# Kernel tuning notes

Hardware: AMD Instinct MI355X
Metric: run time of the kernel (lower is better)

Reference implementation:

```python
import jax, jax.numpy as jnp
import numpy as np

S = 4096   # sequence length == max_length
L = 16     # CHAR_LENGTH
F = 256    # char feature size == word-embed size (hidden_size kwarg)
H = 512    # LSTM hidden = 2 * hidden_size kwarg
V = 44     # char vocab from build_char_lang()


def setup_inputs() -> dict:
    key = jax.random.key(0)
    ks = jax.random.split(key, 12)
    def rn(k, shape, s=0.05):
        return jax.random.normal(k, shape, jnp.float32) * s
    return {
        "word_embeddings": rn(ks[0], (S, F), 1.0),
        "char_idxs": jax.random.randint(ks[1], (S, L), 0, V),
        "char_embed": rn(ks[2], (V, F), 1.0),
        "conv_w": rn(ks[3], (F, 2, F)),           # [out_ch, kh=2, kw=F]
        "conv_b": jnp.zeros((F,), jnp.float32),
        "lin_w": rn(ks[4], (F, F)),
        "lin_b": jnp.zeros((F,), jnp.float32),
        "Wih_f": rn(ks[5], (4 * H, H)),
        "Whh_f": rn(ks[6], (4 * H, H)),
        "bih_f": jnp.zeros((4 * H,), jnp.float32),
        "bhh_f": jnp.zeros((4 * H,), jnp.float32),
        "Wih_r": rn(ks[7], (4 * H, H)),
        "Whh_r": rn(ks[8], (4 * H, H)),
        "bih_r": jnp.zeros((4 * H,), jnp.float32),
        "bhh_r": jnp.zeros((4 * H,), jnp.float32),
    }


def _lstm(x, Wih, Whh, bih, bhh):
    """PyTorch-convention single-layer LSTM over leading axis of x [T, H]."""
    Hh = Whh.shape[1]
    b = bih + bhh
    def step(carry, xt):
        h, c = carry
        g = xt @ Wih.T + h @ Whh.T + b          # [4H]
        i, f, gg, o = jnp.split(g, 4)
        c = jax.nn.sigmoid(f) * c + jax.nn.sigmoid(i) * jnp.tanh(gg)
        h = jax.nn.sigmoid(o) * jnp.tanh(c)
        return (h, c), h
    z = jnp.zeros((Hh,), x.dtype)
    (h, c), ys = jax.lax.scan(step, (z, z), x)
    return ys, h, c


def _char_cnn(char_idxs, char_embed, conv_w, conv_b, lin_w, lin_b):
    ce = char_embed[char_idxs]                          # [S, L, F]
    win = jnp.stack([ce[:, :-1, :], ce[:, 1:, :]], 2)    # [S, L-1, 2, F]
    conv = jnp.einsum('slkf,okf->slo', win, conv_w) + conv_b  # [S, L-1, F]
    pooled = jnp.max(jax.nn.relu(conv), axis=1)          # maxpool over L-1 -> [S, F]
    return pooled @ lin_w.T + lin_b                      # [S, F]


def reference(word_embeddings, char_idxs, char_embed, conv_w, conv_b, lin_w, lin_b,
              Wih_f, Whh_f, bih_f, bhh_f, Wih_r, Whh_r, bih_r, bhh_r):
    char_feat = _char_cnn(char_idxs, char_embed, conv_w, conv_b, lin_w, lin_b)
    x = jnp.concatenate([word_embeddings, char_feat], axis=1)   # [S, H]
    fwd_out, hf, cf = _lstm(x, Wih_f, Whh_f, bih_f, bhh_f)
    rev_out, hr, cr = _lstm(x[::-1], Wih_r, Whh_r, bih_r, bhh_r)
    outputs = jnp.concatenate([fwd_out, rev_out[::-1]], axis=1)  # [S, 2H]
    hidden = jnp.concatenate([hf, hr])                           # [2H]
    cell = jnp.concatenate([cf, cr])                             # [2H]
    return outputs, hidden, cell
```

## Files before the change

### kernel.cpp

```cpp
#include <hip/hip_runtime.h>
#include <cstdint>

#define SQ 4096
#define FD 256
#define HD 512
#define GD 2048

#define WS_X       0
#define WS_XPROJ   (WS_X + SQ*HD)
#define WS_WT      (WS_XPROJ + 2*SQ*GD)
#define WS_LINT    (WS_WT + 2*FD*FD)
#define WS_SYNC    (WS_LINT + FD*FD)

typedef __attribute__((ext_vector_type(4))) float f32x4;
typedef unsigned long long u64;

__device__ __forceinline__ float sigf(float x) { return 1.f / (1.f + __expf(-x)); }

#define REP32(M) M(0)M(1)M(2)M(3)M(4)M(5)M(6)M(7)M(8)M(9)M(10)M(11)M(12)M(13)M(14)M(15) \
                 M(16)M(17)M(18)M(19)M(20)M(21)M(22)M(23)M(24)M(25)M(26)M(27)M(28)M(29)M(30)M(31)

__global__ __launch_bounds__(256) void prep_kernel(const float* __restrict__ conv_w,
                                                   const float* __restrict__ lin_w,
                                                   float* __restrict__ Wt,
                                                   float* __restrict__ linT,
                                                   float* __restrict__ sync) {
  int n = blockIdx.x * 256 + threadIdx.x;
  if (n < 4096) sync[n] = 0.f;
  if (n < 2 * FD * FD) {
    int o = n & 255, f = (n >> 8) & 255, k = n >> 16;
    Wt[n] = conv_w[o * 512 + k * 256 + f];
  } else {
    int m = n - 2 * FD * FD;
    int o = m & 255, f = m >> 8;
    linT[m] = lin_w[o * 256 + f];
  }
}

__global__ __launch_bounds__(256) void charcnn_kernel(const float* __restrict__ wemb,
    const int* __restrict__ cidx, const float* __restrict__ cemb,
    const float* __restrict__ Wt, const float* __restrict__ conv_b,
    const float* __restrict__ linT, const float* __restrict__ lin_b,
    float* __restrict__ x) {
  __shared__ float ceT[256][20];
  __shared__ float pooled[256];
  int s = blockIdx.x, o = threadIdx.x;
  #pragma unroll
  for (int l = 0; l < 16; ++l) {
    int idx = cidx[s * 16 + l];
    ceT[o][l] = cemb[idx * 256 + o];
  }
  __syncthreads();
  float acc[15];
  float cb = conv_b[o];
  #pragma unroll
  for (int l = 0; l < 15; ++l) acc[l] = cb;
  for (int f = 0; f < 256; ++f) {
    float w0 = Wt[f * 256 + o];
    float w1 = Wt[65536 + f * 256 + o];
    float4 ca = *(const float4*)&ceT[f][0];
    float4 cv = *(const float4*)&ceT[f][4];
    float4 cc = *(const float4*)&ceT[f][8];
    float4 cd = *(const float4*)&ceT[f][12];
    float c[16] = {ca.x, ca.y, ca.z, ca.w, cv.x, cv.y, cv.z, cv.w,
                   cc.x, cc.y, cc.z, cc.w, cd.x, cd.y, cd.z, cd.w};
    #pragma unroll
    for (int l = 0; l < 15; ++l) acc[l] += c[l] * w0 + c[l + 1] * w1;
  }
  float m = 0.f;
  #pragma unroll
  for (int l = 0; l < 15; ++l) m = fmaxf(m, acc[l]);
  pooled[o] = m;
  __syncthreads();
  float a2 = lin_b[o];
  for (int f = 0; f < 256; f += 4) {
    float4 p = *(const float4*)&pooled[f];
    a2 += p.x * linT[(f + 0) * 256 + o] + p.y * linT[(f + 1) * 256 + o]
        + p.z * linT[(f + 2) * 256 + o] + p.w * linT[(f + 3) * 256 + o];
  }
  x[(size_t)s * 512 + o] = wemb[(size_t)s * 256 + o];
  x[(size_t)s * 512 + 256 + o] = a2;
}

__global__ __launch_bounds__(256) void xproj_kernel(const float* __restrict__ x,
    const float* __restrict__ Wih_f, const float* __restrict__ Wih_r,
    const float* __restrict__ bih_f, const float* __restrict__ bhh_f,
    const float* __restrict__ bih_r, const float* __restrict__ bhh_r,
    float* __restrict__ xproj) {
  __shared__ float As[64][33];
  __shared__ float Bs[64][33];
  int dir = blockIdx.z;
  const float* B  = dir ? Wih_r : Wih_f;
  const float* b1 = dir ? bih_r : bih_f;
  const float* b2 = dir ? bhh_r : bhh_f;
  int m0 = blockIdx.x * 64, n0 = blockIdx.y * 64;
  int tid = threadIdx.x, tx = tid & 15, ty = tid >> 4;
  float acc[4][4];
  #pragma unroll
  for (int j = 0; j < 4; ++j) {
    float bias = b1[n0 + tx * 4 + j] + b2[n0 + tx * 4 + j];
    #pragma unroll
    for (int i = 0; i < 4; ++i) acc[i][j] = bias;
  }
  int lc = tid & 31, lr0 = tid >> 5;
  for (int k0 = 0; k0 < 512; k0 += 32) {
    #pragma unroll
    for (int i = 0; i < 8; ++i) {
      As[lr0 + 8 * i][lc] = x[(size_t)(m0 + lr0 + 8 * i) * 512 + k0 + lc];
      Bs[lr0 + 8 * i][lc] = B[(size_t)(n0 + lr0 + 8 * i) * 512 + k0 + lc];
    }
    __syncthreads();
    #pragma unroll
    for (int kk = 0; kk < 32; ++kk) {
      float a0 = As[ty * 4 + 0][kk], a1 = As[ty * 4 + 1][kk];
      float a2 = As[ty * 4 + 2][kk], a3 = As[ty * 4 + 3][kk];
      float q0 = Bs[tx * 4 + 0][kk], q1 = Bs[tx * 4 + 1][kk];
      float q2 = Bs[tx * 4 + 2][kk], q3 = Bs[tx * 4 + 3][kk];
      acc[0][0] += a0 * q0; acc[0][1] += a0 * q1; acc[0][2] += a0 * q2; acc[0][3] += a0 * q3;
      acc[1][0] += a1 * q0; acc[1][1] += a1 * q1; acc[1][2] += a1 * q2; acc[1][3] += a1 * q3;
      acc[2][0] += a2 * q0; acc[2][1] += a2 * q1; acc[2][2] += a2 * q2; acc[2][3] += a2 * q3;
      acc[3][0] += a3 * q0; acc[3][1] += a3 * q1; acc[3][2] += a3 * q2; acc[3][3] += a3 * q3;
    }
    __syncthreads();
  }
  size_t base = (size_t)dir * SQ * GD;
  #pragma unroll
  for (int i = 0; i < 4; ++i) {
    float4 v = make_float4(acc[i][0], acc[i][1], acc[i][2], acc[i][3]);
    *(float4*)&xproj[base + (size_t)(m0 + ty * 4 + i) * GD + n0 + tx * 4] = v;
  }
}

__global__ __launch_bounds__(512, 2) void lstm_kernel(const float* __restrict__ xproj,
    const float* __restrict__ Whh_f, const float* __restrict__ Whh_r,
    u64* __restrict__ payu, float* __restrict__ out) {
  __shared__ float h4[4 * 132];
  __shared__ float g_lds[128];
  int dir = blockIdx.x >> 4;
  int wid = blockIdx.x & 15;
  int hbase = wid * 32;
  int tid = threadIdx.x;

  int r = tid >> 2, kq = tid & 3;
  int Rrow = ((r >> 5) << 9) + hbase + (r & 31);
  const float* Whh = dir ? Whh_r : Whh_f;
  const float* xp = xproj + (size_t)dir * SQ * GD;
  const f32x4* wsrc4 = (const f32x4*)(Whh + (size_t)Rrow * 512 + kq * 128);
#define LDW(i) f32x4 w##i = wsrc4[i];
  REP32(LDW)
#undef LDW

  int ib = tid >> 4, ic = tid & 15;
  float cst = 0.f, hlast = 0.f;

  for (int t = 0; t < SQ; ++t) {
    int p = dir ? (SQ - 1 - t) : t;
    float xval = 0.f;
    if (kq == 0) xval = xp[(size_t)p * GD + Rrow];
    if (tid < 256) {
      float v0, v1;
      if (t == 0) { v0 = 0.f; v1 = 0.f; }
      else {
        const u64* src = payu + ((((size_t)dir * 2 + ((t - 1) & 1)) * 16 + ib) * 16 + ic) * 2;
        unsigned tg = (unsigned)t;
        for (;;) {
          u64 lo = __hip_atomic_load(src,     __ATOMIC_RELAXED, __HIP_MEMORY_SCOPE_AGENT);
          u64 hi = __hip_atomic_load(src + 1, __ATOMIC_RELAXED, __HIP_MEMORY_SCOPE_AGENT);
          if ((unsigned)lo == tg && (unsigned)(hi >> 32) == tg) {
            v0 = __uint_as_float((unsigned)(lo >> 32));
            v1 = __uint_as_float((unsigned)hi);
            break;
          }
          __builtin_amdgcn_s_sleep(1);
        }
      }
      int ih = ib * 32 + ic * 2;
      h4[(ih >> 7) * 132 + (ih & 127)] = v0;
      int ih1 = ih + 1;
      h4[(ih1 >> 7) * 132 + (ih1 & 127)] = v1;
    }
    __syncthreads();
    float a0 = 0.f, a1 = 0.f, a2 = 0.f, a3 = 0.f;
    const f32x4* hq4 = (const f32x4*)&h4[kq * 132];
#define GST(i) { f32x4 hh = hq4[i]; \
    a0 = fmaf(w##i[0], hh[0], a0); a1 = fmaf(w##i[1], hh[1], a1); \
    a2 = fmaf(w##i[2], hh[2], a2); a3 = fmaf(w##i[3], hh[3], a3); }
    REP32(GST)
#undef GST
    float acc = (a0 + a1) + (a2 + a3);
    acc += __shfl_xor(acc, 1);
    acc += __shfl_xor(acc, 2);
    if (kq == 0) g_lds[r] = acc + xval;
    __syncthreads();
    if (tid < 32) {
      float ig = g_lds[tid], fg = g_lds[32 + tid], gg = g_lds[64 + tid], og = g_lds[96 + tid];
      float c = sigf(fg) * cst + sigf(ig) * tanhf(gg);
      float hval = sigf(og) * tanhf(c);
      cst = c; hlast = hval;
      out[(size_t)p * 1024 + dir * 512 + hbase + tid] = hval;
      unsigned tg = (unsigned)(t + 1);
      u64 word = (tid & 1) ? (((u64)tg << 32) | __float_as_uint(hval))
                           : (((u64)__float_as_uint(hval) << 32) | tg);
      u64* dst = payu + ((((size_t)dir * 2 + (t & 1)) * 16 + wid) * 16 + (tid >> 1)) * 2 + (tid & 1);
      __hip_atomic_store(dst, word, __ATOMIC_RELAXED, __HIP_MEMORY_SCOPE_AGENT);
    }
  }
  if (tid < 32) {
    size_t OH = (size_t)SQ * 1024;
    out[OH + dir * 512 + hbase + tid] = hlast;
    out[OH + 1024 + dir * 512 + hbase + tid] = cst;
  }
}

extern "C" void kernel_launch(void* const* d_in, const int* in_sizes, int n_in,
                              void* d_out, int out_size, void* d_ws, size_t ws_size,
                              hipStream_t stream) {
  const float* wemb   = (const float*)d_in[0];
  const int*   cidx   = (const int*)d_in[1];
  const float* cemb   = (const float*)d_in[2];
  const float* conv_w = (const float*)d_in[3];
  const float* conv_b = (const float*)d_in[4];
  const float* lin_w  = (const float*)d_in[5];
  const float* lin_b  = (const float*)d_in[6];
  const float* Wih_f  = (const float*)d_in[7];
  const float* Whh_f  = (const float*)d_in[8];
  const float* bih_f  = (const float*)d_in[9];
  const float* bhh_f  = (const float*)d_in[10];
  const float* Wih_r  = (const float*)d_in[11];
  const float* Whh_r  = (const float*)d_in[12];
  const float* bih_r  = (const float*)d_in[13];
  const float* bhh_r  = (const float*)d_in[14];
  float* out = (float*)d_out;
  float* ws = (float*)d_ws;
  float* x     = ws + WS_X;
  float* xproj = ws + WS_XPROJ;
  float* Wt    = ws + WS_WT;
  float* linT  = ws + WS_LINT;
  float* sync  = ws + WS_SYNC;

  prep_kernel<<<768, 256, 0, stream>>>(conv_w, lin_w, Wt, linT, sync);
  charcnn_kernel<<<SQ, 256, 0, stream>>>(wemb, cidx, cemb, Wt, conv_b, linT, lin_b, x);
  xproj_kernel<<<dim3(64, 32, 2), 256, 0, stream>>>(x, Wih_f, Wih_r, bih_f, bhh_f, bih_r, bhh_r, xproj);
  lstm_kernel<<<32, 512, 0, stream>>>(xproj, Whh_f, Whh_r, (u64*)sync, out);
}
```

Before: 8.594 ms.

## Replicate LSTM hidden-state mailbox per reader and split gate activations across lanes

Each producer block now writes its hidden-state words into 16 per-reader copies of the mailbox instead of one, so the reading blocks poll distinct cache lines rather than all contending on the same ones. The sleep in the poll loop is removed, mailbox addresses are precomputed outside the time loop, and the weight loads use inline assembly followed by an explicit wait. The gate nonlinearities are spread over 64 lanes with shuffles to shorten the serial tail of each step. The cost is 16 times more atomic stores per step, a larger sync region to zero, and busier spinning that may consume memory bandwidth.

```diff
diff --git a/kernel.cpp b/kernel.cpp
--- a/kernel.cpp
+++ b/kernel.cpp
@@ -26,7 +26,7 @@
                                                    float* __restrict__ linT,
                                                    float* __restrict__ sync) {
   int n = blockIdx.x * 256 + threadIdx.x;
-  if (n < 4096) sync[n] = 0.f;
+  if (n < 65536) sync[n] = 0.f;
   if (n < 2 * FD * FD) {
     int o = n & 255, f = (n >> 8) & 255, k = n >> 16;
     Wt[n] = conv_w[o * 512 + k * 256 + f];
@@ -146,11 +146,22 @@
   const float* Whh = dir ? Whh_r : Whh_f;
   const float* xp = xproj + (size_t)dir * SQ * GD;
   const f32x4* wsrc4 = (const f32x4*)(Whh + (size_t)Rrow * 512 + kq * 128);
-#define LDW(i) f32x4 w##i = wsrc4[i];
+#define LDW(i) f32x4 w##i; \
+  asm volatile("global_load_dwordx4 %0, %1, off offset:%2" \
+               : "=v"(w##i) : "v"(wsrc4), "i"(16 * i));
   REP32(LDW)
 #undef LDW
+  asm volatile("s_waitcnt vmcnt(0)" ::: "memory");
+  __builtin_amdgcn_sched_barrier(0);
 
   int ib = tid >> 4, ic = tid & 15;
+  size_t rd_off = (((size_t)wid * 16 + ib) * 16 + ic) * 2;
+  const u64* rd_base0 = payu + (size_t)(dir * 2 + 0) * 8192 + rd_off;
+  const u64* rd_base1 = payu + (size_t)(dir * 2 + 1) * 8192 + rd_off;
+  size_t wr_off = ((size_t)wid * 16 + (tid >> 1)) * 2 + (tid & 1);
+  u64* wr_base0 = payu + (size_t)(dir * 2 + 0) * 8192 + wr_off;
+  u64* wr_base1 = payu + (size_t)(dir * 2 + 1) * 8192 + wr_off;
+
   float cst = 0.f, hlast = 0.f;
 
   for (int t = 0; t < SQ; ++t) {
@@ -161,7 +172,7 @@
       float v0, v1;
       if (t == 0) { v0 = 0.f; v1 = 0.f; }
       else {
-        const u64* src = payu + ((((size_t)dir * 2 + ((t - 1) & 1)) * 16 + ib) * 16 + ic) * 2;
+        const u64* src = ((t - 1) & 1) ? rd_base1 : rd_base0;
         unsigned tg = (unsigned)t;
         for (;;) {
           u64 lo = __hip_atomic_load(src,     __ATOMIC_RELAXED, __HIP_MEMORY_SCOPE_AGENT);
@@ -171,7 +182,6 @@
             v1 = __uint_as_float((unsigned)hi);
             break;
           }
-          __builtin_amdgcn_s_sleep(1);
         }
       }
       int ih = ib * 32 + ic * 2;
@@ -192,17 +202,28 @@
     acc += __shfl_xor(acc, 2);
     if (kq == 0) g_lds[r] = acc + xval;
     __syncthreads();
-    if (tid < 32) {
-      float ig = g_lds[tid], fg = g_lds[32 + tid], gg = g_lds[64 + tid], og = g_lds[96 + tid];
-      float c = sigf(fg) * cst + sigf(ig) * tanhf(gg);
-      float hval = sigf(og) * tanhf(c);
-      cst = c; hlast = hval;
-      out[(size_t)p * 1024 + dir * 512 + hbase + tid] = hval;
-      unsigned tg = (unsigned)(t + 1);
-      u64 word = (tid & 1) ? (((u64)tg << 32) | __float_as_uint(hval))
-                           : (((u64)__float_as_uint(hval) << 32) | tg);
-      u64* dst = payu + ((((size_t)dir * 2 + (t & 1)) * 16 + wid) * 16 + (tid >> 1)) * 2 + (tid & 1);
-      __hip_atomic_store(dst, word, __ATOMIC_RELAXED, __HIP_MEMORY_SCOPE_AGENT);
+    if (tid < 64) {
+      int j = tid & 31;
+      bool hiw = tid >= 32;
+      float vA = hiw ? g_lds[64 + j] : g_lds[j];
+      float vB = hiw ? g_lds[96 + j] : g_lds[32 + j];
+      float aA = hiw ? tanhf(vA) : sigf(vA);
+      float aB = sigf(vB);
+      float bA = __shfl_xor(aA, 32);
+      float bB = __shfl_xor(aB, 32);
+      if (!hiw) {
+        float c = aB * cst + aA * bA;
+        float hval = bB * tanhf(c);
+        cst = c; hlast = hval;
+        unsigned tg = (unsigned)(t + 1);
+        u64 word = (tid & 1) ? (((u64)tg << 32) | __float_as_uint(hval))
+                             : (((u64)__float_as_uint(hval) << 32) | tg);
+        u64* wb = (t & 1) ? wr_base1 : wr_base0;
+        #pragma unroll
+        for (int rd = 0; rd < 16; ++rd)
+          __hip_atomic_store(wb + (size_t)rd * 512, word, __ATOMIC_RELAXED, __HIP_MEMORY_SCOPE_AGENT);
+        out[(size_t)p * 1024 + dir * 512 + hbase + tid] = hval;
+      }
     }
   }
   if (tid < 32) {
```

After: 10.54 ms. +22.6%, slower.

## Restructure LSTM step: per-lane gate mapping, shuffle gate gather, double-buffered h

Applied to the files above, without the earlier changes.

Remaps threads so each hidden unit's four gates sit in one wave, letting gate values be gathered with shuffles instead of an LDS round trip and a second barrier. It double-buffers the h vector in shared memory, publishes one tagged 64-bit word per hidden unit, and has all 512 threads poll without sleep. It also swaps tanhf for a fast exp-based approximation. Whh weights are now reloaded from global/L2 inside every timestep instead of being held in registers, which adds memory traffic per step.

```diff
diff --git a/kernel.cpp b/kernel.cpp
--- a/kernel.cpp
+++ b/kernel.cpp
@@ -16,6 +16,11 @@
 typedef unsigned long long u64;
 
 __device__ __forceinline__ float sigf(float x) { return 1.f / (1.f + __expf(-x)); }
+__device__ __forceinline__ float tanhf_fast(float x) {
+  float xx = fminf(15.f, fmaxf(-15.f, x));
+  float e = __expf(2.f * xx);
+  return (e - 1.f) * __frcp_rn(e + 1.f);
+}
 
 #define REP32(M) M(0)M(1)M(2)M(3)M(4)M(5)M(6)M(7)M(8)M(9)M(10)M(11)M(12)M(13)M(14)M(15) \
                  M(16)M(17)M(18)M(19)M(20)M(21)M(22)M(23)M(24)M(25)M(26)M(27)M(28)M(29)M(30)M(31)
@@ -134,54 +139,46 @@
 __global__ __launch_bounds__(512, 2) void lstm_kernel(const float* __restrict__ xproj,
     const float* __restrict__ Whh_f, const float* __restrict__ Whh_r,
     u64* __restrict__ payu, float* __restrict__ out) {
-  __shared__ float h4[4 * 132];
-  __shared__ float g_lds[128];
+  __shared__ float h4[2][4 * 132];
   int dir = blockIdx.x >> 4;
   int wid = blockIdx.x & 15;
   int hbase = wid * 32;
   int tid = threadIdx.x;
-
-  int r = tid >> 2, kq = tid & 3;
-  int Rrow = ((r >> 5) << 9) + hbase + (r & 31);
+  int w = tid >> 6, l = tid & 63;
+  int jl = l >> 4, gate = (l >> 2) & 3, kq = l & 3;
+  int j = w * 4 + jl;
+  int Rrow = (gate << 9) + hbase + j;
   const float* Whh = dir ? Whh_r : Whh_f;
   const float* xp = xproj + (size_t)dir * SQ * GD;
   const f32x4* wsrc4 = (const f32x4*)(Whh + (size_t)Rrow * 512 + kq * 128);
-#define LDW(i) f32x4 w##i = wsrc4[i];
-  REP32(LDW)
-#undef LDW
-
-  int ib = tid >> 4, ic = tid & 15;
+  u64* mypay = payu + dir * 1024;
+  const bool gl = (l & 15) == 0;
+  const bool xl = (l & 3) == 0;
+  const int qoff = (tid >> 7) * 132 + (tid & 127);
+  const int base = l & 48;
   float cst = 0.f, hlast = 0.f;
 
   for (int t = 0; t < SQ; ++t) {
     int p = dir ? (SQ - 1 - t) : t;
+#define LDW(i) f32x4 w##i = wsrc4[i];
+    REP32(LDW)
+#undef LDW
     float xval = 0.f;
-    if (kq == 0) xval = xp[(size_t)p * GD + Rrow];
-    if (tid < 256) {
-      float v0, v1;
-      if (t == 0) { v0 = 0.f; v1 = 0.f; }
-      else {
-        const u64* src = payu + ((((size_t)dir * 2 + ((t - 1) & 1)) * 16 + ib) * 16 + ic) * 2;
-        unsigned tg = (unsigned)t;
-        for (;;) {
-          u64 lo = __hip_atomic_load(src,     __ATOMIC_RELAXED, __HIP_MEMORY_SCOPE_AGENT);
-          u64 hi = __hip_atomic_load(src + 1, __ATOMIC_RELAXED, __HIP_MEMORY_SCOPE_AGENT);
-          if ((unsigned)lo == tg && (unsigned)(hi >> 32) == tg) {
-            v0 = __uint_as_float((unsigned)(lo >> 32));
-            v1 = __uint_as_float((unsigned)hi);
-            break;
-          }
-          __builtin_amdgcn_s_sleep(1);
-        }
-      }
-      int ih = ib * 32 + ic * 2;
-      h4[(ih >> 7) * 132 + (ih & 127)] = v0;
-      int ih1 = ih + 1;
-      h4[(ih1 >> 7) * 132 + (ih1 & 127)] = v1;
+    if (xl) xval = xp[(size_t)p * GD + Rrow];
+    float* hbuf = h4[t & 1];
+    if (t == 0) {
+      hbuf[qoff] = 0.f;
+    } else {
+      const u64* src = mypay + ((t - 1) & 1) * 512 + tid;
+      unsigned tg = (unsigned)t;
+      u64 v;
+      do { v = __hip_atomic_load(src, __ATOMIC_RELAXED, __HIP_MEMORY_SCOPE_AGENT); }
+      while ((unsigned)(v >> 32) != tg);
+      hbuf[qoff] = __uint_as_float((unsigned)v);
     }
     __syncthreads();
     float a0 = 0.f, a1 = 0.f, a2 = 0.f, a3 = 0.f;
-    const f32x4* hq4 = (const f32x4*)&h4[kq * 132];
+    const f32x4* hq4 = (const f32x4*)&hbuf[kq * 132];
 #define GST(i) { f32x4 hh = hq4[i]; \
     a0 = fmaf(w##i[0], hh[0], a0); a1 = fmaf(w##i[1], hh[1], a1); \
     a2 = fmaf(w##i[2], hh[2], a2); a3 = fmaf(w##i[3], hh[3], a3); }
@@ -190,25 +187,25 @@
     float acc = (a0 + a1) + (a2 + a3);
     acc += __shfl_xor(acc, 1);
     acc += __shfl_xor(acc, 2);
-    if (kq == 0) g_lds[r] = acc + xval;
-    __syncthreads();
-    if (tid < 32) {
-      float ig = g_lds[tid], fg = g_lds[32 + tid], gg = g_lds[64 + tid], og = g_lds[96 + tid];
-      float c = sigf(fg) * cst + sigf(ig) * tanhf(gg);
-      float hval = sigf(og) * tanhf(c);
+    float gx = acc + xval;
+    float sI = __shfl(gx, base);
+    float sF = __shfl(gx, base | 4);
+    float sG = __shfl(gx, base | 8);
+    float sO = __shfl(gx, base | 12);
+    if (gl) {
+      float c = sigf(sF) * cst + sigf(sI) * tanhf_fast(sG);
+      float hval = sigf(sO) * tanhf_fast(c);
       cst = c; hlast = hval;
-      out[(size_t)p * 1024 + dir * 512 + hbase + tid] = hval;
-      unsigned tg = (unsigned)(t + 1);
-      u64 word = (tid & 1) ? (((u64)tg << 32) | __float_as_uint(hval))
-                           : (((u64)__float_as_uint(hval) << 32) | tg);
-      u64* dst = payu + ((((size_t)dir * 2 + (t & 1)) * 16 + wid) * 16 + (tid >> 1)) * 2 + (tid & 1);
-      __hip_atomic_store(dst, word, __ATOMIC_RELAXED, __HIP_MEMORY_SCOPE_AGENT);
-    }
-  }
-  if (tid < 32) {
+      u64 word = ((u64)(unsigned)(t + 1) << 32) | __float_as_uint(hval);
+      __hip_atomic_store(mypay + (t & 1) * 512 + hbase + j, word,
+                         __ATOMIC_RELAXED, __HIP_MEMORY_SCOPE_AGENT);
+      out[(size_t)p * 1024 + dir * 512 + hbase + j] = hval;
+    }
+  }
+  if (gl) {
     size_t OH = (size_t)SQ * 1024;
-    out[OH + dir * 512 + hbase + tid] = hlast;
-    out[OH + 1024 + dir * 512 + hbase + tid] = cst;
+    out[OH + dir * 512 + hbase + j] = hlast;
+    out[OH + 1024 + dir * 512 + hbase + j] = cst;
   }
 }
 
```

Result: slower. 9.833 ms (+14.4%).
